# Kernel optimization log

Hardware: AMD Instinct MI355X
Metric: run time of the kernel (lower is better)

The kernel has to match this reference:

```python
import jax, jax.numpy as jnp
import numpy as np

N = 50000      # nodes
E = 300000     # edges
F_IN = 128     # num_features
H = 256        # hidden_dim
C = 32         # num_classes


def gcn_conv(x, src, dst, W, b, num_nodes):
    """PyG-style GCNConv: add self-loops, sym-normalize, X W, scatter-add, + bias."""
    loop = jnp.arange(num_nodes, dtype=src.dtype)
    src2 = jnp.concatenate([src, loop])          # [E+N]
    dst2 = jnp.concatenate([dst, loop])          # [E+N]
    # degree of target nodes (with self-loops, unit edge weights)
    deg = jax.ops.segment_sum(jnp.ones_like(dst2, dtype=x.dtype), dst2,
                              num_segments=num_nodes)
    dinv = jnp.where(deg > 0, jax.lax.rsqrt(deg), 0.0)
    norm = dinv[src2] * dinv[dst2]               # [E+N]
    h = x @ W                                    # [N, out]  dense GEMM first (PyG order)
    msg = h[src2] * norm[:, None]                # gather + scale  [E+N, out]
    out = jax.ops.segment_sum(msg, dst2, num_segments=num_nodes)  # scatter-add
    return out + b


def setup_inputs() -> dict:
    key = jax.random.key(0)
    ks = jax.random.split(key, 8)
    x = jax.random.normal(ks[0], (N, F_IN), dtype=jnp.float32)
    edge_index = jax.random.randint(ks[1], (2, E), 0, N, dtype=jnp.int64)
    W1 = jax.random.normal(ks[2], (F_IN, H), dtype=jnp.float32) / np.float32(np.sqrt(F_IN))
    b1 = jnp.zeros((H,), jnp.float32)
    W2 = jax.random.normal(ks[3], (H, H), dtype=jnp.float32) / np.float32(np.sqrt(H))
    b2 = jnp.zeros((H,), jnp.float32)
    Wc = jax.random.normal(ks[4], (H, C), dtype=jnp.float32) / np.float32(np.sqrt(H))
    bc = jnp.zeros((C,), jnp.float32)
    return {"x": x, "edge_index": edge_index, "W1": W1, "b1": b1,
            "W2": W2, "b2": b2, "Wc": Wc, "bc": bc}


def reference(x, edge_index, W1, b1, W2, b2, Wc, bc):
    src, dst = edge_index[0], edge_index[1]
    h = gcn_conv(x, src, dst, W1, b1, N)
    h = jax.nn.relu(h)                 # dropout is identity in eval mode
    h = gcn_conv(h, src, dst, W2, b2, N)
    h = jax.nn.relu(h)
    return h @ Wc + bc                 # [N, C]
```

## Files before the change

### kernel.cpp

```cpp
#include <hip/hip_runtime.h>
#include <math.h>

using short8 = __attribute__((ext_vector_type(8))) short;
using f32x4 = __attribute__((ext_vector_type(4))) float;

#define CAP 48

__device__ inline short f2bf(float f) {
    unsigned u = __builtin_bit_cast(unsigned, f);
    unsigned r = (u + 0x7fffu + ((u >> 16) & 1u)) >> 16;
    return (short)r;
}
__device__ inline float bf2f(short s) {
    unsigned u = ((unsigned)(unsigned short)s) << 16;
    return __builtin_bit_cast(float, u);
}

typedef const void __attribute__((address_space(1))) gvoid_t;
typedef void __attribute__((address_space(3))) svoid_t;
__device__ inline void gload16(const short* g, short* l) {
    __builtin_amdgcn_global_load_lds((gvoid_t*)g, (svoid_t*)l, 16, 0, 0);
}


__global__ void prep_kernel(const float* __restrict__ x, const float* __restrict__ W1,
                            const float* __restrict__ W2, const float* __restrict__ Wc,
                            const int* __restrict__ src, const int* __restrict__ dst,
                            short* __restrict__ xb, short* __restrict__ Wt1,
                            short* __restrict__ Wt2, short* __restrict__ Wtc,
                            int* __restrict__ deg, int* __restrict__ eslot,
                            int n, int e) {
    int idx = blockIdx.x * blockDim.x + threadIdx.x;
    const int nx8 = n * 16;
    if (idx < nx8) {
        const float4* p = (const float4*)x + (size_t)idx * 2;
        float4 v0 = p[0], v1 = p[1];
        short8 o;
        o[0] = f2bf(v0.x); o[1] = f2bf(v0.y); o[2] = f2bf(v0.z); o[3] = f2bf(v0.w);
        o[4] = f2bf(v1.x); o[5] = f2bf(v1.y); o[6] = f2bf(v1.z); o[7] = f2bf(v1.w);
        ((short8*)xb)[idx] = o;
        return;
    }
    idx -= nx8;
    if (idx < 128 * 256) {
        int k = idx >> 8, c = idx & 255;
        Wt1[c * 128 + k] = f2bf(W1[idx]);
        return;
    }
    idx -= 128 * 256;
    if (idx < 256 * 256) {
        int k = idx >> 8, c = idx & 255;
        Wt2[c * 256 + k] = f2bf(W2[idx]);
        return;
    }
    idx -= 256 * 256;
    if (idx < 256 * 32) {
        int k = idx >> 5, c = idx & 31;
        Wtc[c * 256 + k] = f2bf(Wc[idx]);
        return;
    }
    idx -= 256 * 32;
    if (idx < e) {
        int d = dst[idx], s = src[idx];
        int pos = atomicAdd(&deg[d], 1);
        if (pos < CAP) eslot[(size_t)d * CAP + pos] = s;
    }
}


template<bool RELU_BF16OUT>
__global__ __launch_bounds__(256) void mfma_gemm128_kernel(
    const short* __restrict__ A, const short* __restrict__ Wt,
    const float* __restrict__ bias, void* __restrict__ Cout,
    int M, int K, int NC)
{
    __shared__ short As[128 * 32];
    __shared__ short Bs[128 * 32];

    const int tid = threadIdx.x;
    const int wave = tid >> 6, lane = tid & 63;
    const int m0 = blockIdx.y * 128, n0 = blockIdx.x * 128;
    const int wm = (wave >> 1) * 64, wn = (wave & 1) * 64;

    const int lr0 = tid >> 2;
    const int lr1 = 64 + lr0;
    const int cdst = tid & 3;
    const int cg0 = cdst ^ ((lr0 >> 1) & 3);
    const int cg1 = cdst ^ ((lr1 >> 1) & 3);
    int ga0 = m0 + lr0; if (ga0 >= M) ga0 = M - 1;
    int ga1 = m0 + lr1; if (ga1 >= M) ga1 = M - 1;
    int gb0 = n0 + lr0; if (gb0 >= NC) gb0 = NC - 1;
    int gb1 = n0 + lr1; if (gb1 >= NC) gb1 = NC - 1;
    const short* pa0 = A + (size_t)ga0 * K + cg0 * 8;
    const short* pa1 = A + (size_t)ga1 * K + cg1 * 8;
    const short* pb0 = Wt + (size_t)gb0 * K + cg0 * 8;
    const short* pb1 = Wt + (size_t)gb1 * K + cg1 * 8;

    short* lA0 = &As[(wave * 16) * 32];
    short* lA1 = &As[(64 + wave * 16) * 32];
    short* lB0 = &Bs[(wave * 16) * 32];
    short* lB1 = &Bs[(64 + wave * 16) * 32];

    f32x4 acc[4][4] = {};
    const int fr = lane & 15;
    const int cfrag = lane >> 4;
    const int swzr = (fr >> 1) & 3;

    for (int k0 = 0; k0 < K; k0 += 32) {
        gload16(pa0 + k0, lA0);
        gload16(pa1 + k0, lA1);
        gload16(pb0 + k0, lB0);
        gload16(pb1 + k0, lB1);
        __syncthreads();

        short8 af[4], bfv[4];
        #pragma unroll
        for (int mt = 0; mt < 4; ++mt) {
            int rr = wm + mt * 16 + fr;
            af[mt] = *(const short8*)&As[rr * 32 + ((cfrag ^ swzr) << 3)];
        }
        #pragma unroll
        for (int nt = 0; nt < 4; ++nt) {
            int rr = wn + nt * 16 + fr;
            bfv[nt] = *(const short8*)&Bs[rr * 32 + ((cfrag ^ swzr) << 3)];
        }

        #pragma unroll
        for (int mt = 0; mt < 4; ++mt)
            #pragma unroll
            for (int nt = 0; nt < 4; ++nt)
                acc[mt][nt] = __builtin_amdgcn_mfma_f32_16x16x32_bf16(
                    af[mt], bfv[nt], acc[mt][nt], 0, 0, 0);

        __syncthreads();
    }

    #pragma unroll
    for (int mt = 0; mt < 4; ++mt) {
        #pragma unroll
        for (int nt = 0; nt < 4; ++nt) {
            #pragma unroll
            for (int r = 0; r < 4; ++r) {
                int grow = m0 + wm + mt * 16 + (lane >> 4) * 4 + r;
                int gcol = n0 + wn + nt * 16 + (lane & 15);
                if (grow < M && gcol < NC) {
                    float v = acc[mt][nt][r] + bias[gcol];
                    if (RELU_BF16OUT)
                        ((short*)Cout)[(size_t)grow * NC + gcol] = f2bf(fmaxf(v, 0.f));
                    else
                        ((float*)Cout)[(size_t)grow * NC + gcol] = v;
                }
            }
        }
    }
}


__global__ __launch_bounds__(128) void mfma_gemmc_kernel(
    const short* __restrict__ A, const short* __restrict__ Wt,
    const float* __restrict__ bias, float* __restrict__ Cout,
    int M, int K)
{
    const int NC = 32;
    __shared__ short As[128 * 40];
    __shared__ short Bs[32 * 40];

    const int tid = threadIdx.x;
    const int wave = tid >> 6, lane = tid & 63;
    const int m0 = blockIdx.x * 128;
    const int wm = wave * 64;

    const int sar = tid >> 2;
    const int sak = (tid & 3) * 8;
    int gr0 = m0 + sar;       if (gr0 >= M) gr0 = M - 1;
    int gr1 = m0 + 32 + sar;  if (gr1 >= M) gr1 = M - 1;
    int gr2 = m0 + 64 + sar;  if (gr2 >= M) gr2 = M - 1;
    int gr3 = m0 + 96 + sar;  if (gr3 >= M) gr3 = M - 1;
    const short* pa0 = A + (size_t)gr0 * K + sak;
    const short* pa1 = A + (size_t)gr1 * K + sak;
    const short* pa2 = A + (size_t)gr2 * K + sak;
    const short* pa3 = A + (size_t)gr3 * K + sak;
    const short* pb  = Wt + (size_t)sar * K + sak;

    f32x4 acc[4][2] = {};
    const int fr = lane & 15;
    const int fk = (lane >> 4) * 8;

    for (int k0 = 0; k0 < K; k0 += 32) {
        short8 va0 = *(const short8*)(pa0 + k0);
        short8 va1 = *(const short8*)(pa1 + k0);
        short8 va2 = *(const short8*)(pa2 + k0);
        short8 va3 = *(const short8*)(pa3 + k0);
        short8 vb  = *(const short8*)(pb + k0);
        __syncthreads();
        *(short8*)&As[(sar)       * 40 + sak] = va0;
        *(short8*)&As[(32 + sar)  * 40 + sak] = va1;
        *(short8*)&As[(64 + sar)  * 40 + sak] = va2;
        *(short8*)&As[(96 + sar)  * 40 + sak] = va3;
        *(short8*)&Bs[sar * 40 + sak] = vb;
        __syncthreads();

        short8 af[4], bfv[2];
        #pragma unroll
        for (int mt = 0; mt < 4; ++mt)
            af[mt] = *(const short8*)&As[(wm + mt * 16 + fr) * 40 + fk];
        #pragma unroll
        for (int nt = 0; nt < 2; ++nt)
            bfv[nt] = *(const short8*)&Bs[(nt * 16 + fr) * 40 + fk];

        #pragma unroll
        for (int mt = 0; mt < 4; ++mt)
            #pragma unroll
            for (int nt = 0; nt < 2; ++nt)
                acc[mt][nt] = __builtin_amdgcn_mfma_f32_16x16x32_bf16(
                    af[mt], bfv[nt], acc[mt][nt], 0, 0, 0);
    }

    #pragma unroll
    for (int mt = 0; mt < 4; ++mt) {
        #pragma unroll
        for (int nt = 0; nt < 2; ++nt) {
            #pragma unroll
            for (int r = 0; r < 4; ++r) {
                int grow = m0 + wm + mt * 16 + (lane >> 4) * 4 + r;
                int gcol = nt * 16 + (lane & 15);
                if (grow < M)
                    Cout[(size_t)grow * NC + gcol] = acc[mt][nt][r] + bias[gcol];
            }
        }
    }
}


template<int LPN>
__global__ __launch_bounds__(256) void gather_kernel(
    const short* __restrict__ h, const int* __restrict__ deg,
    const int* __restrict__ eslot, short* __restrict__ out, int n)
{
    const int F = LPN * 8;
    int node = (blockIdx.x * 256 + threadIdx.x) / LPN;
    if (node >= n) return;
    int lane = threadIdx.x % LPN;
    int f = lane * 8;

    int dg = deg[node];
    if (dg > CAP) dg = CAP;
    float di = rsqrtf((float)dg + 1.0f);
    float w = di * di;

    const size_t rb = (size_t)node * F + f;
    short8 hv = *(const short8*)(h + rb);
    float a[8];
    #pragma unroll
    for (int j = 0; j < 8; ++j) a[j] = bf2f(hv[j]) * w;

    const int* bucket = eslot + (size_t)node * CAP;
    for (int e = 0; e < dg; e += 4) {
        int4 s4 = *(const int4*)(bucket + e);
        int i0 = s4.x;
        int i1 = (e + 1 < dg) ? s4.y : 0;
        int i2 = (e + 2 < dg) ? s4.z : 0;
        int i3 = (e + 3 < dg) ? s4.w : 0;
        int d0 = deg[i0], d1 = deg[i1], d2 = deg[i2], d3 = deg[i3];
        short8 v0 = *(const short8*)(h + (size_t)i0 * F + f);
        short8 v1 = *(const short8*)(h + (size_t)i1 * F + f);
        short8 v2 = *(const short8*)(h + (size_t)i2 * F + f);
        short8 v3 = *(const short8*)(h + (size_t)i3 * F + f);
        float w0 = rsqrtf((float)d0 + 1.0f) * di;
        float w1 = (e + 1 < dg) ? rsqrtf((float)d1 + 1.0f) * di : 0.f;
        float w2 = (e + 2 < dg) ? rsqrtf((float)d2 + 1.0f) * di : 0.f;
        float w3 = (e + 3 < dg) ? rsqrtf((float)d3 + 1.0f) * di : 0.f;
        #pragma unroll
        for (int j = 0; j < 8; ++j) {
            a[j] = fmaf(bf2f(v0[j]), w0, a[j]);
            a[j] = fmaf(bf2f(v1[j]), w1, a[j]);
            a[j] = fmaf(bf2f(v2[j]), w2, a[j]);
            a[j] = fmaf(bf2f(v3[j]), w3, a[j]);
        }
    }
    short8 o;
    #pragma unroll
    for (int j = 0; j < 8; ++j) o[j] = f2bf(a[j]);
    *(short8*)(out + rb) = o;
}


extern "C" void kernel_launch(void* const* d_in, const int* in_sizes, int n_in,
                              void* d_out, int out_size, void* d_ws, size_t ws_size,
                              hipStream_t stream) {
    const float* x  = (const float*)d_in[0];
    const int*   ei = (const int*)d_in[1];
    const float* W1 = (const float*)d_in[2];
    const float* b1 = (const float*)d_in[3];
    const float* W2 = (const float*)d_in[4];
    const float* b2 = (const float*)d_in[5];
    const float* Wc = (const float*)d_in[6];
    const float* bc = (const float*)d_in[7];
    float* out = (float*)d_out;

    const int E = in_sizes[1] / 2;
    const int N = in_sizes[0] / 128;
    const int F_IN = 128, H = 256;
    const int* src = ei;
    const int* dst = ei + E;

    short* xb   = (short*)d_ws;
    short* aggX = xb + (size_t)N * 128;
    short* hA   = aggX + (size_t)N * 128;
    short* hB   = hA + (size_t)N * 256;
    short* Wt1  = hB + (size_t)N * 256;
    short* Wt2  = Wt1 + 256 * 128;
    short* Wtc  = Wt2 + 256 * 256;
    int*   deg  = (int*)(Wtc + 32 * 256);
    int*   eslot= deg + N;

    const int TB = 256;

    hipMemsetAsync(deg, 0, (size_t)N * sizeof(int), stream);

    const int prep_total = N * 16 + 128 * 256 + 256 * 256 + 256 * 32 + E;
    prep_kernel<<<(prep_total + TB - 1) / TB, TB, 0, stream>>>(
        x, W1, W2, Wc, src, dst, xb, Wt1, Wt2, Wtc, deg, eslot, N, E);

    const int gy = (N + 127) / 128;

    gather_kernel<16><<<((size_t)N * 16 + TB - 1) / TB, TB, 0, stream>>>(
        xb, deg, eslot, aggX, N);
    mfma_gemm128_kernel<true><<<dim3(H / 128, gy), 256, 0, stream>>>(aggX, Wt1, b1, hA, N, F_IN, H);

    gather_kernel<32><<<((size_t)N * 32 + TB - 1) / TB, TB, 0, stream>>>(
        hA, deg, eslot, hB, N);
    mfma_gemm128_kernel<true><<<dim3(H / 128, gy), 256, 0, stream>>>(hB, Wt2, b2, hA, N, H, H);

    mfma_gemmc_kernel<<<gy, 128, 0, stream>>>(hA, Wtc, bc, out, N, H);
}
```

Baseline: 222.8 us.

## Fuse second GCN GEMM with classifier GEMM, keeping hidden tile in LDS

```diff
diff --git a/kernel.cpp b/kernel.cpp
--- a/kernel.cpp
+++ b/kernel.cpp
@@ -156,77 +156,107 @@
 }
 
 
-__global__ __launch_bounds__(128) void mfma_gemmc_kernel(
-    const short* __restrict__ A, const short* __restrict__ Wt,
-    const float* __restrict__ bias, float* __restrict__ Cout,
-    int M, int K)
+__global__ __launch_bounds__(512) void gemm2c_kernel(
+    const short* __restrict__ A,
+    const short* __restrict__ Wt2,
+    const float* __restrict__ b2,
+    const short* __restrict__ Wtc,
+    const float* __restrict__ bc,
+    float* __restrict__ out,
+    int M)
 {
-    const int NC = 32;
-    __shared__ short As[128 * 40];
-    __shared__ short Bs[32 * 40];
+    const int K = 256;
+    const int TP = 264;
+    __shared__ short smem[128 * 264];
+    short* As = smem;
+    short* Bs = smem + 128 * 32;
 
     const int tid = threadIdx.x;
     const int wave = tid >> 6, lane = tid & 63;
     const int m0 = blockIdx.x * 128;
-    const int wm = wave * 64;
-
-    const int sar = tid >> 2;
-    const int sak = (tid & 3) * 8;
-    int gr0 = m0 + sar;       if (gr0 >= M) gr0 = M - 1;
-    int gr1 = m0 + 32 + sar;  if (gr1 >= M) gr1 = M - 1;
-    int gr2 = m0 + 64 + sar;  if (gr2 >= M) gr2 = M - 1;
-    int gr3 = m0 + 96 + sar;  if (gr3 >= M) gr3 = M - 1;
-    const short* pa0 = A + (size_t)gr0 * K + sak;
-    const short* pa1 = A + (size_t)gr1 * K + sak;
-    const short* pa2 = A + (size_t)gr2 * K + sak;
-    const short* pa3 = A + (size_t)gr3 * K + sak;
-    const short* pb  = Wt + (size_t)sar * K + sak;
-
-    f32x4 acc[4][2] = {};
+    const int wm = (wave >> 2) * 64;
+    const int wn = (wave & 3) * 64;
+
+    const int srow = lane >> 2;
+    const int cdst = lane & 3;
+    const int lrA  = wave * 16 + srow;
+    const int lrB1 = 128 + lrA;
+    int gaA = m0 + lrA; if (gaA >= M) gaA = M - 1;
+    const int cgA  = cdst ^ ((lrA  >> 1) & 3);
+    const int cgB1 = cdst ^ ((lrB1 >> 1) & 3);
+    const short* pa  = A   + (size_t)gaA  * K + cgA  * 8;
+    const short* pb0 = Wt2 + (size_t)lrA  * K + cgA  * 8;
+    const short* pb1 = Wt2 + (size_t)lrB1 * K + cgB1 * 8;
+    short* lA  = &As[(wave * 16) * 32];
+    short* lB0 = &Bs[(wave * 16) * 32];
+    short* lB1 = &Bs[(128 + wave * 16) * 32];
+
+    f32x4 acc[4][4] = {};
     const int fr = lane & 15;
-    const int fk = (lane >> 4) * 8;
+    const int cfrag = lane >> 4;
+    const int swzr = (fr >> 1) & 3;
 
     for (int k0 = 0; k0 < K; k0 += 32) {
-        short8 va0 = *(const short8*)(pa0 + k0);
-        short8 va1 = *(const short8*)(pa1 + k0);
-        short8 va2 = *(const short8*)(pa2 + k0);
-        short8 va3 = *(const short8*)(pa3 + k0);
-        short8 vb  = *(const short8*)(pb + k0);
+        gload16(pa  + k0, lA);
+        gload16(pb0 + k0, lB0);
+        gload16(pb1 + k0, lB1);
         __syncthreads();
-        *(short8*)&As[(sar)       * 40 + sak] = va0;
-        *(short8*)&As[(32 + sar)  * 40 + sak] = va1;
-        *(short8*)&As[(64 + sar)  * 40 + sak] = va2;
-        *(short8*)&As[(96 + sar)  * 40 + sak] = va3;
-        *(short8*)&Bs[sar * 40 + sak] = vb;
-        __syncthreads();
-
-        short8 af[4], bfv[2];
-        #pragma unroll
-        for (int mt = 0; mt < 4; ++mt)
-            af[mt] = *(const short8*)&As[(wm + mt * 16 + fr) * 40 + fk];
-        #pragma unroll
-        for (int nt = 0; nt < 2; ++nt)
-            bfv[nt] = *(const short8*)&Bs[(nt * 16 + fr) * 40 + fk];
+
+        short8 af[4], bfv[4];
+        #pragma unroll
+        for (int mt = 0; mt < 4; ++mt) {
+            int rr = wm + mt * 16 + fr;
+            af[mt] = *(const short8*)&As[rr * 32 + ((cfrag ^ swzr) << 3)];
+        }
+        #pragma unroll
+        for (int nt = 0; nt < 4; ++nt) {
+            int rr = wn + nt * 16 + fr;
+            bfv[nt] = *(const short8*)&Bs[rr * 32 + ((cfrag ^ swzr) << 3)];
+        }
 
         #pragma unroll
         for (int mt = 0; mt < 4; ++mt)
             #pragma unroll
-            for (int nt = 0; nt < 2; ++nt)
+            for (int nt = 0; nt < 4; ++nt)
                 acc[mt][nt] = __builtin_amdgcn_mfma_f32_16x16x32_bf16(
                     af[mt], bfv[nt], acc[mt][nt], 0, 0, 0);
+
+        __syncthreads();
     }
 
     #pragma unroll
     for (int mt = 0; mt < 4; ++mt) {
         #pragma unroll
-        for (int nt = 0; nt < 2; ++nt) {
+        for (int nt = 0; nt < 4; ++nt) {
             #pragma unroll
             for (int r = 0; r < 4; ++r) {
-                int grow = m0 + wm + mt * 16 + (lane >> 4) * 4 + r;
-                int gcol = nt * 16 + (lane & 15);
-                if (grow < M)
-                    Cout[(size_t)grow * NC + gcol] = acc[mt][nt][r] + bias[gcol];
+                int lrow = wm + mt * 16 + (lane >> 4) * 4 + r;
+                int gcol = wn + nt * 16 + fr;
+                float v = acc[mt][nt][r] + b2[gcol];
+                smem[lrow * TP + gcol] = f2bf(fmaxf(v, 0.f));
             }
+        }
+    }
+    __syncthreads();
+
+    f32x4 c2[2] = {};
+    const int fk = (lane >> 4) * 8;
+    for (int k0 = 0; k0 < K; k0 += 32) {
+        short8 a8 = *(const short8*)&smem[(wave * 16 + fr) * TP + fk + k0];
+        #pragma unroll
+        for (int nt = 0; nt < 2; ++nt) {
+            short8 b8 = *(const short8*)(Wtc + (size_t)(nt * 16 + fr) * K + fk + k0);
+            c2[nt] = __builtin_amdgcn_mfma_f32_16x16x32_bf16(a8, b8, c2[nt], 0, 0, 0);
+        }
+    }
+    #pragma unroll
+    for (int nt = 0; nt < 2; ++nt) {
+        #pragma unroll
+        for (int r = 0; r < 4; ++r) {
+            int grow = m0 + wave * 16 + (lane >> 4) * 4 + r;
+            int gcol = nt * 16 + fr;
+            if (grow < M)
+                out[(size_t)grow * 32 + gcol] = c2[nt][r] + bc[gcol];
         }
     }
 }
@@ -330,7 +360,5 @@
 
     gather_kernel<32><<<((size_t)N * 32 + TB - 1) / TB, TB, 0, stream>>>(
         hA, deg, eslot, hB, N);
-    mfma_gemm128_kernel<true><<<dim3(H / 128, gy), 256, 0, stream>>>(hB, Wt2, b2, hA, N, H, H);
-
-    mfma_gemmc_kernel<<<gy, 128, 0, stream>>>(hA, Wtc, bc, out, N, H);
-}
+    gemm2c_kernel<<<gy, 512, 0, stream>>>(hB, Wt2, b2, Wtc, bc, out, N);
+}
```

Result: faster. 203.5 us (-8.7%).
